# Kernel optimization log

Hardware: AMD Instinct MI355X
Metric: run time of the kernel (lower is better)

The kernel has to match this reference:

```python
import jax, jax.numpy as jnp
import numpy as np

D = 4096


def ste_sign(v):
    # forward: sign(v); backward: identity (straight-through)
    return v + jax.lax.stop_gradient(jnp.sign(v) - v)


def setup_inputs() -> dict:
    key = jax.random.key(0)
    ks = jax.random.split(key, 7)
    B, T = 2, 4096
    x = jax.random.normal(ks[0], (B, T, D), dtype=jnp.float32)
    role_write = jax.random.normal(ks[1], (D,), dtype=jnp.float32) * 0.02
    role_read = jax.random.normal(ks[2], (D,), dtype=jnp.float32) * 0.02
    # nn.Linear(D, 1): weight (1, D) stored here as (D,), bias scalar (1,)
    lim = 1.0 / np.sqrt(D)
    wg_w = jax.random.uniform(ks[3], (D,), dtype=jnp.float32, minval=-lim, maxval=lim)
    wg_b = jax.random.uniform(ks[4], (1,), dtype=jnp.float32, minval=-lim, maxval=lim)
    rg_w = jax.random.uniform(ks[5], (D,), dtype=jnp.float32, minval=-lim, maxval=lim)
    rg_b = jax.random.uniform(ks[6], (1,), dtype=jnp.float32, minval=-lim, maxval=lim)
    return {"x": x, "role_write": role_write, "role_read": role_read,
            "wg_w": wg_w, "wg_b": wg_b, "rg_w": rg_w, "rg_b": rg_b}


def reference(x, role_write, role_read, wg_w, wg_b, rg_w, rg_b):
    # ---- write: gated sign-bind facts, causal bundle via cumsum over T ----
    signs = ste_sign(x)                                  # (B,T,D)
    facts = signs * ste_sign(role_write)                 # bind with write role
    w_gate = jax.nn.sigmoid(jnp.einsum('btd,d->bt', x, wg_w) + wg_b[0])
    gated_facts = facts * w_gate[..., None]
    memory = jnp.cumsum(gated_facts, axis=1)             # (B,T,D) causal bundle
    # ---- read: unbind memory with query, gated residual add ----
    query = signs * ste_sign(role_read)
    retrieved = ste_sign(memory) * query
    r_gate = jax.nn.sigmoid(jnp.einsum('btd,d->bt', x, rg_w) + rg_b[0])
    return x + r_gate[..., None] * retrieved
```

## Files before the change

### kernel.cpp

```cpp
#include <hip/hip_runtime.h>
#include <math.h>


#define T_LEN 4096
#define D_LEN 4096
#define TC 32
#define NC (T_LEN / TC)
#define D4 (D_LEN / 4)

typedef float nfloat4 __attribute__((ext_vector_type(4)));

__device__ __forceinline__ float fsgn(float v) {
    return (v > 0.f) ? 1.f : ((v < 0.f) ? -1.f : 0.f);
}
__device__ __forceinline__ double dsgn(double v) {
    return (v > 0.) ? 1. : ((v < 0.) ? -1. : 0.);
}
__device__ __forceinline__ unsigned scode(float v) {
    return (v > 0.f) ? 2u : ((v < 0.f) ? 0u : 1u);
}

__global__ __launch_bounds__(256) void gates_pack_kernel(
    const float* __restrict__ x,
    const float* __restrict__ wg_w, const float* __restrict__ wg_b,
    const float* __restrict__ rg_w, const float* __restrict__ rg_b,
    double* __restrict__ wgate, double* __restrict__ rgate,
    unsigned char* __restrict__ packed)
{
    const int row = blockIdx.x;
    const float4* xr = (const float4*)(x + (size_t)row * D_LEN);
    const float4* w4 = (const float4*)wg_w;
    const float4* r4 = (const float4*)rg_w;
    unsigned char* pr = packed + (size_t)row * D4;

    double dw = 0., dr = 0.;
    #pragma unroll 4
    for (int i = threadIdx.x; i < D4; i += 256) {
        float4 v = xr[i];
        float4 a = w4[i];
        float4 g = r4[i];
        dw += (double)v.x * a.x + (double)v.y * a.y
            + (double)v.z * a.z + (double)v.w * a.w;
        dr += (double)v.x * g.x + (double)v.y * g.y
            + (double)v.z * g.z + (double)v.w * g.w;
        pr[i] = (unsigned char)(scode(v.x) | (scode(v.y) << 2)
                              | (scode(v.z) << 4) | (scode(v.w) << 6));
    }
    for (int off = 32; off > 0; off >>= 1) {
        dw += __shfl_down(dw, off);
        dr += __shfl_down(dr, off);
    }
    __shared__ double sdw[4], sdr[4];
    const int wid = threadIdx.x >> 6;
    if ((threadIdx.x & 63) == 0) { sdw[wid] = dw; sdr[wid] = dr; }
    __syncthreads();
    if (threadIdx.x == 0) {
        double zw = sdw[0] + sdw[1] + sdw[2] + sdw[3] + (double)wg_b[0];
        double zr = sdr[0] + sdr[1] + sdr[2] + sdr[3] + (double)rg_b[0];
        wgate[row] = 1. / (1. + exp(-zw));
        rgate[row] = 1. / (1. + exp(-zr));
    }
}

__global__ __launch_bounds__(256) void partial_kernel(
    const unsigned char* __restrict__ packed,
    const double* __restrict__ wgate,
    double* __restrict__ partial)
{
    const int c = blockIdx.x;
    const int b = blockIdx.y;
    const int tid = threadIdx.x;

    __shared__ double wsm[TC];
    if (tid < TC) wsm[tid] = wgate[b * T_LEN + c * TC + tid];
    __syncthreads();

    double acc[16];
    #pragma unroll
    for (int k = 0; k < 16; ++k) acc[k] = 0.;

    const size_t rowbase = ((size_t)b * T_LEN + (size_t)c * TC) * D4;
    for (int t = 0; t < TC; ++t) {
        unsigned pk = *(const unsigned*)(packed + rowbase + (size_t)t * D4 + tid * 4);
        double w = wsm[t];
        #pragma unroll
        for (int k = 0; k < 16; ++k) {
            int code = (int)((pk >> (2 * k)) & 3u) - 1;
            acc[k] += (double)code * w;
        }
    }
    double* p = partial + ((size_t)(b * NC + c)) * D_LEN + tid * 16;
    #pragma unroll
    for (int k = 0; k < 16; ++k) p[k] = acc[k];
}

__global__ __launch_bounds__(256) void prefix_kernel(
    const double* __restrict__ partial, double* __restrict__ prefix)
{
    const int m = blockIdx.x * 256 + threadIdx.x;
    const int b = blockIdx.y;
    double s = 0.;
    for (int c = 0; c < NC; ++c) {
        size_t idx = ((size_t)(b * NC + c)) * D_LEN + m;
        double v = partial[idx];
        prefix[idx] = s;
        s += v;
    }
}

__global__ __launch_bounds__(256) void final_kernel(
    const float* __restrict__ x,
    const double* __restrict__ wgate, const double* __restrict__ rgate,
    const float* __restrict__ role_w, const float* __restrict__ role_r,
    const double* __restrict__ prefix,
    float* __restrict__ out)
{
    const int b = blockIdx.z;
    const int c = blockIdx.y;
    const int d4 = blockIdx.x * 256 + threadIdx.x;

    __shared__ double wsm[TC];
    __shared__ float rsm[TC];
    if (threadIdx.x < TC) {
        wsm[threadIdx.x] = wgate[b * T_LEN + c * TC + threadIdx.x];
        rsm[threadIdx.x] = (float)rgate[b * T_LEN + c * TC + threadIdx.x];
    }
    __syncthreads();

    float4 rw = ((const float4*)role_w)[d4];
    float4 rr = ((const float4*)role_r)[d4];
    const float kx = fsgn(rw.x) * fsgn(rr.x);
    const float ky = fsgn(rw.y) * fsgn(rr.y);
    const float kz = fsgn(rw.z) * fsgn(rr.z);
    const float kw = fsgn(rw.w) * fsgn(rr.w);

    const double* p = prefix + ((size_t)(b * NC + c)) * D_LEN + d4 * 4;
    double ax = p[0], ay = p[1], az = p[2], aw = p[3];

    const float4* x4 = (const float4*)x;
    nfloat4* o4 = (nfloat4*)out;
    const size_t slab = ((size_t)b * T_LEN + (size_t)c * TC) * D4 + d4;

    #pragma unroll 4
    for (int i = 0; i < TC; ++i) {
        float4 v = x4[slab + (size_t)i * D4];
        double w = wsm[i];
        float rf = rsm[i];
        float sx = fsgn(v.x), sy = fsgn(v.y), sz = fsgn(v.z), sw2 = fsgn(v.w);
        ax += (double)sx * w; ay += (double)sy * w;
        az += (double)sz * w; aw += (double)sw2 * w;
        nfloat4 o;
        o.x = v.x + rf * kx * (float)dsgn(ax) * sx;
        o.y = v.y + rf * ky * (float)dsgn(ay) * sy;
        o.z = v.z + rf * kz * (float)dsgn(az) * sz;
        o.w = v.w + rf * kw * (float)dsgn(aw) * sw2;
        __builtin_nontemporal_store(o, &o4[slab + (size_t)i * D4]);
    }
}

extern "C" void kernel_launch(void* const* d_in, const int* in_sizes, int n_in,
                              void* d_out, int out_size, void* d_ws, size_t ws_size,
                              hipStream_t stream) {
    const float* x      = (const float*)d_in[0];
    const float* role_w = (const float*)d_in[1];
    const float* role_r = (const float*)d_in[2];
    const float* wg_w   = (const float*)d_in[3];
    const float* wg_b   = (const float*)d_in[4];
    const float* rg_w   = (const float*)d_in[5];
    const float* rg_b   = (const float*)d_in[6];
    float* out = (float*)d_out;

    const int B = in_sizes[0] / (T_LEN * D_LEN);
    const int BT = B * T_LEN;

    double* wgate   = (double*)d_ws;
    double* rgate   = wgate + BT;
    double* partial = rgate + BT;
    double* prefix  = partial + (size_t)B * NC * D_LEN;
    unsigned char* packed = (unsigned char*)(prefix + (size_t)B * NC * D_LEN);

    gates_pack_kernel<<<BT, 256, 0, stream>>>(
        x, wg_w, wg_b, rg_w, rg_b, wgate, rgate, packed);

    dim3 g2a(NC, B);
    partial_kernel<<<g2a, 256, 0, stream>>>(packed, wgate, partial);

    dim3 g2b(D_LEN / 256, B);
    prefix_kernel<<<g2b, 256, 0, stream>>>(partial, prefix);

    dim3 g3(D4 / 256, NC, B);
    final_kernel<<<g3, 256, 0, stream>>>(
        x, wgate, rgate, role_w, role_r, prefix, out);
}
```

Baseline: 95.61 us.

## Fuse gate computation and chunk partial sums into one kernel via LDS

Merges the gates/pack kernel and the partial-sum kernel into one 1024-thread block per 32-row chunk. Sign codes stay in shared memory instead of going through a global packed buffer, and each 32-lane group reduces one row's gate dot products. This drops one launch and the global write and reread of the packed codes. In exchange the grid shrinks to 256 large blocks with 32KB of LDS each, which may lower parallelism for the x-streaming phase.

```diff
diff --git a/kernel.cpp b/kernel.cpp
--- a/kernel.cpp
+++ b/kernel.cpp
@@ -20,78 +20,70 @@
     return (v > 0.f) ? 2u : ((v < 0.f) ? 0u : 1u);
 }
 
-__global__ __launch_bounds__(256) void gates_pack_kernel(
+__global__ __launch_bounds__(1024) void gates_partial_kernel(
     const float* __restrict__ x,
     const float* __restrict__ wg_w, const float* __restrict__ wg_b,
     const float* __restrict__ rg_w, const float* __restrict__ rg_b,
     double* __restrict__ wgate, double* __restrict__ rgate,
-    unsigned char* __restrict__ packed)
-{
-    const int row = blockIdx.x;
-    const float4* xr = (const float4*)(x + (size_t)row * D_LEN);
-    const float4* w4 = (const float4*)wg_w;
-    const float4* r4 = (const float4*)rg_w;
-    unsigned char* pr = packed + (size_t)row * D4;
-
-    double dw = 0., dr = 0.;
-    #pragma unroll 4
-    for (int i = threadIdx.x; i < D4; i += 256) {
-        float4 v = xr[i];
-        float4 a = w4[i];
-        float4 g = r4[i];
-        dw += (double)v.x * a.x + (double)v.y * a.y
-            + (double)v.z * a.z + (double)v.w * a.w;
-        dr += (double)v.x * g.x + (double)v.y * g.y
-            + (double)v.z * g.z + (double)v.w * g.w;
-        pr[i] = (unsigned char)(scode(v.x) | (scode(v.y) << 2)
-                              | (scode(v.z) << 4) | (scode(v.w) << 6));
-    }
-    for (int off = 32; off > 0; off >>= 1) {
-        dw += __shfl_down(dw, off);
-        dr += __shfl_down(dr, off);
-    }
-    __shared__ double sdw[4], sdr[4];
-    const int wid = threadIdx.x >> 6;
-    if ((threadIdx.x & 63) == 0) { sdw[wid] = dw; sdr[wid] = dr; }
-    __syncthreads();
-    if (threadIdx.x == 0) {
-        double zw = sdw[0] + sdw[1] + sdw[2] + sdw[3] + (double)wg_b[0];
-        double zr = sdr[0] + sdr[1] + sdr[2] + sdr[3] + (double)rg_b[0];
-        wgate[row] = 1. / (1. + exp(-zw));
-        rgate[row] = 1. / (1. + exp(-zr));
-    }
-}
-
-__global__ __launch_bounds__(256) void partial_kernel(
-    const unsigned char* __restrict__ packed,
-    const double* __restrict__ wgate,
     double* __restrict__ partial)
 {
     const int c = blockIdx.x;
     const int b = blockIdx.y;
     const int tid = threadIdx.x;
 
-    __shared__ double wsm[TC];
-    if (tid < TC) wsm[tid] = wgate[b * T_LEN + c * TC + tid];
+    __shared__ unsigned char codes[TC][D4];
+    __shared__ double wg_s[TC];
+    __shared__ double rg_s[TC];
+
+    const int r  = tid >> 5;
+    const int k0 = tid & 31;
+    const float4* xr = (const float4*)(x + ((size_t)b * T_LEN + (size_t)c * TC + r) * D_LEN);
+    const float4* w4 = (const float4*)wg_w;
+    const float4* g4 = (const float4*)rg_w;
+
+    double dw = 0., dg = 0.;
+    #pragma unroll 4
+    for (int j = 0; j < 32; ++j) {
+        const int idx = k0 + j * 32;
+        float4 v = xr[idx];
+        float4 a = w4[idx];
+        float4 g = g4[idx];
+        dw += (double)v.x * a.x + (double)v.y * a.y
+            + (double)v.z * a.z + (double)v.w * a.w;
+        dg += (double)v.x * g.x + (double)v.y * g.y
+            + (double)v.z * g.z + (double)v.w * g.w;
+        codes[r][idx] = (unsigned char)(scode(v.x) | (scode(v.y) << 2)
+                                      | (scode(v.z) << 4) | (scode(v.w) << 6));
+    }
+    #pragma unroll
+    for (int off = 16; off >= 1; off >>= 1) {
+        dw += __shfl_down(dw, off, 32);
+        dg += __shfl_down(dg, off, 32);
+    }
+    if (k0 == 0) {
+        wg_s[r] = 1. / (1. + exp(-(dw + (double)wg_b[0])));
+        rg_s[r] = 1. / (1. + exp(-(dg + (double)rg_b[0])));
+    }
     __syncthreads();
 
-    double acc[16];
-    #pragma unroll
-    for (int k = 0; k < 16; ++k) acc[k] = 0.;
+    if (tid < TC) {
+        const int row = b * T_LEN + c * TC + tid;
+        wgate[row] = wg_s[tid];
+        rgate[row] = rg_s[tid];
+    }
 
-    const size_t rowbase = ((size_t)b * T_LEN + (size_t)c * TC) * D4;
+    double a0 = 0., a1 = 0., a2 = 0., a3 = 0.;
+    #pragma unroll 8
     for (int t = 0; t < TC; ++t) {
-        unsigned pk = *(const unsigned*)(packed + rowbase + (size_t)t * D4 + tid * 4);
-        double w = wsm[t];
-        #pragma unroll
-        for (int k = 0; k < 16; ++k) {
-            int code = (int)((pk >> (2 * k)) & 3u) - 1;
-            acc[k] += (double)code * w;
-        }
+        unsigned code = codes[t][tid];
+        double w = wg_s[t];
+        a0 += (double)((int)( code       & 3u) - 1) * w;
+        a1 += (double)((int)((code >> 2) & 3u) - 1) * w;
+        a2 += (double)((int)((code >> 4) & 3u) - 1) * w;
+        a3 += (double)((int)((code >> 6) & 3u) - 1) * w;
     }
-    double* p = partial + ((size_t)(b * NC + c)) * D_LEN + tid * 16;
-    #pragma unroll
-    for (int k = 0; k < 16; ++k) p[k] = acc[k];
+    double* rec = partial + ((size_t)(b * NC + c)) * D_LEN + tid * 4;
+    rec[0] = a0; rec[1] = a1; rec[2] = a2; rec[3] = a3;
 }
 
 __global__ __launch_bounds__(256) void prefix_kernel(
@@ -177,13 +169,10 @@
     double* rgate   = wgate + BT;
     double* partial = rgate + BT;
     double* prefix  = partial + (size_t)B * NC * D_LEN;
-    unsigned char* packed = (unsigned char*)(prefix + (size_t)B * NC * D_LEN);
 
-    gates_pack_kernel<<<BT, 256, 0, stream>>>(
-        x, wg_w, wg_b, rg_w, rg_b, wgate, rgate, packed);
-
-    dim3 g2a(NC, B);
-    partial_kernel<<<g2a, 256, 0, stream>>>(packed, wgate, partial);
+    dim3 g12(NC, B);
+    gates_partial_kernel<<<g12, 1024, 0, stream>>>(
+        x, wg_w, wg_b, rg_w, rg_b, wgate, rgate, partial);
 
     dim3 g2b(D_LEN / 256, B);
     prefix_kernel<<<g2b, 256, 0, stream>>>(partial, prefix);
```

New measurement: 88.82 us. 1.08x faster.
